# Performance work log

Measured on AMD Instinct MI355X. Metric: run time of the kernel, lower is better.

The kernel has to match this reference:

```python
import jax, jax.numpy as jnp
import numpy as np

B, T, D = 4, 4096, 1024

def setup_inputs() -> dict:
    key = jax.random.key(0)
    kx, kq, kk, kv = jax.random.split(key, 4)
    s = 1.0 / np.sqrt(D)
    return {
        "x": jax.random.normal(kx, (B, T, D), dtype=jnp.float32),
        "Wq": jax.random.normal(kq, (D, D), dtype=jnp.float32) * s,
        "Wk": jax.random.normal(kk, (D, D), dtype=jnp.float32) * s,
        "Wv": jax.random.normal(kv, (D, D), dtype=jnp.float32) * s,
    }

def reference(x, Wq, Wk, Wv):
    # x: [B, T, D]; W*: [D, D] (torch Linear weight, y = x @ W.T)
    Q = jnp.einsum("btd,ed->bte", x, Wq)
    K = jnp.einsum("btd,ed->bte", x, Wk)
    V = jnp.einsum("btd,ed->bte", x, Wv)
    scale = jnp.asarray(np.sqrt(D), dtype=x.dtype)
    scores = jnp.einsum("bqd,bkd->bqk", Q, K) / scale  # [B, T, T]
    weights = jax.nn.softmax(scores, axis=-1)
    return jnp.einsum("bqk,bkd->bqd", weights, V)
```

## Files before the change

### kernel.cpp

```cpp
#include <hip/hip_runtime.h>
#include <stdint.h>

typedef unsigned short u16;
typedef __attribute__((ext_vector_type(4))) float f32x4;
typedef __attribute__((ext_vector_type(8))) short s16x8;

#define TB 4
#define TT 4096
#define TD 1024

__device__ __forceinline__ u16 f2bf(float f) {
  union { float f; uint32_t u; } v; v.f = f;
  return (u16)((v.u + 0x7FFFu + ((v.u >> 16) & 1u)) >> 16);
}

#define GLOAD_LDS16(g, l) __builtin_amdgcn_global_load_lds( \
    (const __attribute__((address_space(1))) void*)(g),      \
    (__attribute__((address_space(3))) void*)(l), 16, 0, 0)

#define MFMA16(a, b, c) __builtin_amdgcn_mfma_f32_16x16x32_bf16(a, b, c, 0, 0, 0)
#define LDSV(o) (*(const s16x8*)&ls[(o)])

__global__ void cast_all(const float* __restrict__ x, const float* __restrict__ wq,
                         const float* __restrict__ wk, const float* __restrict__ wv,
                         u16* __restrict__ dst) {
  const int NX = 1 << 22;
  const int NW = 1 << 18;
  const int NT = NX + 3 * NW;
  int i = blockIdx.x * blockDim.x + threadIdx.x;
  int stride = gridDim.x * blockDim.x;
  for (; i < NT; i += stride) {
    float4 v;
    if (i < NX) {
      v = ((const float4*)x)[i];
    } else {
      int j = i - NX;
      int w = j >> 18;
      int off = j & (NW - 1);
      const float* p = (w == 0) ? wq : (w == 1) ? wk : wv;
      v = ((const float4*)p)[off];
    }
    ushort4 o;
    o.x = f2bf(v.x); o.y = f2bf(v.y); o.z = f2bf(v.z); o.w = f2bf(v.w);
    ((ushort4*)dst)[i] = o;
  }
}

__global__ void zero_l(float* __restrict__ L) {
  ((float4*)L)[blockIdx.x * 256 + threadIdx.x] = (float4){0.f, 0.f, 0.f, 0.f};
}

template<int EPI>
__global__ __launch_bounds__(512)
void gemm256(const u16* __restrict__ Abase, const u16* __restrict__ Bt,
             void* __restrict__ C, float* __restrict__ L,
             int K, int lda, int ldb, int ldc,
             float s0, float s1,
             size_t oA0, size_t oA1, size_t oA2, size_t oA3, size_t sB,
             size_t oC0, size_t oC1, size_t oC2, size_t oC3) {
  __shared__ u16 ls[65536];
  const int tid  = threadIdx.x;
  const int lane = tid & 63;
  const int wid  = tid >> 6;
  const int wm   = wid >> 2;
  const int wn   = wid & 3;

  const int nxy = gridDim.x * gridDim.y;
  const int id  = blockIdx.y * gridDim.x + blockIdx.x;
  const int sid = (id & 7) * (nxy >> 3) + (id >> 3);
  const int bx  = sid % gridDim.x;
  const int by  = sid / gridDim.x;
  const int brow = by * 256;
  const int bcol = bx * 256;

  const int z = blockIdx.z;
  const size_t oA = (z == 0) ? oA0 : (z == 1) ? oA1 : (z == 2) ? oA2 : oA3;
  const size_t oC = (z == 0) ? oC0 : (z == 1) ? oC1 : (z == 2) ? oC2 : oC3;
  const float scale = (z == 0) ? s0 : s1;
  const u16* A = Abase + oA;
  Bt += (size_t)z * sB;

  const int lr = lane >> 3;
  const int lc = (lane & 7) ^ lr;

  auto SBLK = [&](int slotB, int kt, int op, int r0) {
    const u16* g = op ? (Bt + (size_t)bcol * ldb) : (A + (size_t)brow * lda);
    const int ld = op ? ldb : lda;
    const int r  = r0 + wid * 8 + lr;
    GLOAD_LDS16(g + (size_t)r * ld + (size_t)kt * 64 + (size_t)lc * 8,
                &ls[slotB + op * 16384 + (r0 + wid * 8) * 64]);
  };
  auto SHALF = [&](int slotB, int kt, int op, int h) {
    SBLK(slotB, kt, op, h * 128);
    SBLK(slotB, kt, op, h * 128 + 64);
  };

  f32x4 acc[8][4];
#pragma unroll
  for (int m = 0; m < 8; ++m)
#pragma unroll
    for (int n = 0; n < 4; ++n) acc[m][n] = (f32x4){0.f, 0.f, 0.f, 0.f};

  const int nt = K >> 6;
  const int NI = nt >> 1;

  SHALF(0, 0, 0, 0); SHALF(0, 0, 0, 1);
  SHALF(0, 0, 1, 0); SHALF(0, 0, 1, 1);
  SHALF(32768, 1, 1, 0); SHALF(32768, 1, 1, 1);
  asm volatile("s_waitcnt vmcnt(4)" ::: "memory");
  __builtin_amdgcn_s_barrier();

  const int r16 = lane & 15;
  const int k8  = lane >> 4;
  const int sw  = r16 & 7;
  const int c0  = ((k8)     ^ sw) * 8;
  const int c1  = ((4 | k8) ^ sw) * 8;
  int aBase[8], bBase[4];
#pragma unroll
  for (int m = 0; m < 8; ++m) aBase[m] = (wm * 128 + m * 16 + r16) * 64;
#pragma unroll
  for (int n = 0; n < 4; ++n) bBase[n] = 16384 + (wn * 64 + n * 16 + r16) * 64;

  s16x8 af[4][2], bf[4][2];

#define READ_A4(SB, MH)                                                        \
  af[0][0] = LDSV((SB) + aBase[(MH)*4+0] + c0); af[0][1] = LDSV((SB) + aBase[(MH)*4+0] + c1); \
  af[1][0] = LDSV((SB) + aBase[(MH)*4+1] + c0); af[1][1] = LDSV((SB) + aBase[(MH)*4+1] + c1); \
  af[2][0] = LDSV((SB) + aBase[(MH)*4+2] + c0); af[2][1] = LDSV((SB) + aBase[(MH)*4+2] + c1); \
  af[3][0] = LDSV((SB) + aBase[(MH)*4+3] + c0); af[3][1] = LDSV((SB) + aBase[(MH)*4+3] + c1);

#define READ_B2(SB, N0)                                                        \
  bf[(N0)  ][0] = LDSV((SB) + bBase[(N0)  ] + c0); bf[(N0)  ][1] = LDSV((SB) + bBase[(N0)  ] + c1); \
  bf[(N0)+1][0] = LDSV((SB) + bBase[(N0)+1] + c0); bf[(N0)+1][1] = LDSV((SB) + bBase[(N0)+1] + c1);

#define CLUST(MH, NH)                                                          \
  __builtin_amdgcn_s_setprio(1);                                               \
  _Pragma("unroll")                                                            \
  for (int mm = 0; mm < 4; ++mm) {                                             \
    _Pragma("unroll")                                                          \
    for (int nn = 0; nn < 2; ++nn) {                                           \
      acc[(MH)*4+mm][(NH)*2+nn] =                                              \
          MFMA16(af[mm][0], bf[(NH)*2+nn][0], acc[(MH)*4+mm][(NH)*2+nn]);      \
      acc[(MH)*4+mm][(NH)*2+nn] =                                              \
          MFMA16(af[mm][1], bf[(NH)*2+nn][1], acc[(MH)*4+mm][(NH)*2+nn]);      \
    }                                                                          \
  }                                                                            \
  __builtin_amdgcn_s_setprio(0);

#define PIN() __builtin_amdgcn_sched_barrier(0)
#define BAR() __builtin_amdgcn_s_barrier()

  for (int i = 0; i < NI; ++i) {
    const int t1 = 2 * i + 1, t2 = 2 * i + 2, t3 = 2 * i + 3;
    const bool p2 = t2 < nt, p3 = t3 < nt;

    READ_A4(0, 0); READ_B2(0, 0);
    SHALF(32768, t1, 0, 0);
    PIN(); BAR();
    CLUST(0, 0);
    BAR();

    READ_B2(0, 2);
    SHALF(32768, t1, 0, 1);
    PIN(); BAR();
    CLUST(0, 1);
    BAR();

    READ_A4(0, 1);
    if (p2) SHALF(0, t2, 1, 0);
    PIN(); BAR();
    CLUST(1, 0);
    BAR();

    if (p2) SHALF(0, t2, 1, 1);
    PIN(); BAR();
    CLUST(1, 1);
    if (p2) asm volatile("s_waitcnt vmcnt(4)" ::: "memory");
    else    asm volatile("s_waitcnt vmcnt(0)" ::: "memory");
    BAR();

    READ_A4(32768, 0); READ_B2(32768, 0);
    if (p2) SHALF(0, t2, 0, 0);
    PIN(); BAR();
    CLUST(0, 0);
    BAR();

    READ_B2(32768, 2);
    if (p2) SHALF(0, t2, 0, 1);
    PIN(); BAR();
    CLUST(0, 1);
    BAR();

    READ_A4(32768, 1);
    if (p3) SHALF(32768, t3, 1, 0);
    PIN(); BAR();
    CLUST(1, 0);
    BAR();

    if (p3) SHALF(32768, t3, 1, 1);
    PIN(); BAR();
    CLUST(1, 1);
    if (i + 1 < NI) asm volatile("s_waitcnt vmcnt(4)" ::: "memory");
    BAR();
  }
#undef READ_A4
#undef READ_B2
#undef CLUST
#undef PIN
#undef BAR

  const int c16 = lane & 15;
  const int rhi = lane >> 4;
#pragma unroll
  for (int m = 0; m < 8; ++m) {
#pragma unroll
    for (int r = 0; r < 4; ++r) {
      const int grow = brow + wm * 128 + m * 16 + rhi * 4 + r;
      if (EPI == 1) {
        float vs[4];
        float s = 0.f;
#pragma unroll
        for (int n = 0; n < 4; ++n) {
          vs[n] = __expf(acc[m][n][r] * scale);
          s += vs[n];
        }
#pragma unroll
        for (int n = 0; n < 4; ++n) {
          int gcol = bcol + wn * 64 + n * 16 + c16;
          ((u16*)C)[oC + (size_t)grow * ldc + gcol] = f2bf(vs[n]);
        }
#pragma unroll
        for (int off = 1; off < 16; off <<= 1) s += __shfl_xor(s, off);
        if (c16 == 0) atomicAdd(&L[(size_t)z * 4096 + grow], s);
      } else if (EPI == 2) {
        const float inv = 1.0f / L[(size_t)z * 4096 + grow];
#pragma unroll
        for (int n = 0; n < 4; ++n) {
          int gcol = bcol + wn * 64 + n * 16 + c16;
          ((float*)C)[oC + (size_t)grow * ldc + gcol] = acc[m][n][r] * scale * inv;
        }
      } else {
#pragma unroll
        for (int n = 0; n < 4; ++n) {
          int gcol = bcol + wn * 64 + n * 16 + c16;
          ((u16*)C)[oC + (size_t)grow * ldc + gcol] = f2bf(acc[m][n][r] * scale);
        }
      }
    }
  }
}

__global__ __launch_bounds__(256)
void transpose_bf16(const u16* __restrict__ V, u16* __restrict__ Vt) {
  __shared__ u16 tile[64][65];
  int b  = blockIdx.z;
  int t0 = blockIdx.y * 64;
  int e0 = blockIdx.x * 64;
  const u16* Vb  = V  + (size_t)b * TT * TD;
  u16*       Vtb = Vt + (size_t)b * TT * TD;
  int r  = threadIdx.x >> 4;
  int c4 = threadIdx.x & 15;
#pragma unroll
  for (int i = 0; i < 4; ++i) {
    int row = r + i * 16;
    ushort4 v = *(const ushort4*)&Vb[(size_t)(t0 + row) * TD + e0 + c4 * 4];
    tile[row][c4 * 4 + 0] = v.x;
    tile[row][c4 * 4 + 1] = v.y;
    tile[row][c4 * 4 + 2] = v.z;
    tile[row][c4 * 4 + 3] = v.w;
  }
  __syncthreads();
#pragma unroll
  for (int i = 0; i < 4; ++i) {
    int e = r + i * 16;
    ushort4 o;
    o.x = tile[c4 * 4 + 0][e];
    o.y = tile[c4 * 4 + 1][e];
    o.z = tile[c4 * 4 + 2][e];
    o.w = tile[c4 * 4 + 3][e];
    *(ushort4*)&Vtb[(size_t)(e0 + e) * TT + t0 + c4 * 4] = o;
  }
}

extern "C" void kernel_launch(void* const* d_in, const int* in_sizes, int n_in,
                              void* d_out, int out_size, void* d_ws, size_t ws_size,
                              hipStream_t stream) {
  const float* x  = (const float*)d_in[0];
  const float* Wq = (const float*)d_in[1];
  const float* Wk = (const float*)d_in[2];
  const float* Wv = (const float*)d_in[3];
  float* out = (float*)d_out;

  const size_t MT = (size_t)TB * TT;
  const size_t BE = (size_t)TT * TD;
  const size_t XE = MT * TD;
  const size_t WE = (size_t)TD * TD;

  u16* xb   = (u16*)d_ws;
  u16* wqb  = xb + XE;
  u16* Q    = wqb + 3 * WE;
  u16* Kb   = Q + XE;
  u16* Vt   = Kb + XE;
  u16* PB   = Vt + XE;
  u16* tmpS = PB + 2 * XE;
  float* L  = (float*)wqb;

  cast_all<<<2048, 256, 0, stream>>>(x, Wq, Wk, Wv, xb);

  dim3 blk(512);
  gemm256<0><<<dim3(TD / 256, MT / 256, 3), blk, 0, stream>>>(
      xb, wqb, Q, L, TD, TD, TD, TD, 0.03125f, 1.0f,
      0, 0, 0, 0, WE,
      0, XE, (size_t)(PB - Q), 0);

  transpose_bf16<<<dim3(TD / 64, TT / 64, TB), 256, 0, stream>>>(PB, Vt);

  zero_l<<<16, 256, 0, stream>>>(L);

  gemm256<1><<<dim3(TT / 256, TT / 256, TB), blk, 0, stream>>>(
      Q, Kb, xb, L, TD, TD, TD, TT, 1.0f, 1.0f,
      0, BE, 2 * BE, 3 * BE, BE,
      0, (size_t)(PB - xb), (size_t)(PB + XE - xb), (size_t)(tmpS - xb));

  gemm256<2><<<dim3(TD / 256, TT / 256, TB), blk, 0, stream>>>(
      xb, Vt, out, L, TT, TT, TT, TD, 1.0f, 1.0f,
      0, (size_t)(PB - xb), (size_t)(PB + XE - xb), (size_t)(tmpS - xb), BE,
      0, BE, 2 * BE, 3 * BE);
}
```

Baseline: 418.2 us.

## Compute V transposed directly via swapped GEMM and add LDS waitcnt hints

Replaces the V projection followed by a separate bf16 transpose kernel with a GEMM that computes Wv·xᵀ directly into the transposed Vt layout, one batch per grid z. This removes the transpose launch and the write and re-read of the intermediate V buffer. It also inserts explicit lgkmcnt(8) waits before the barriers in the main loop to order the LDS reads against the compute clusters. The swapped-operand GEMM must produce a correct layout through its offsets, and the extra waits could add stalls.

Result: no change. 420.0 us (median of 3 runs) (+0.4%).

```diff
diff --git a/kernel.cpp b/kernel.cpp
--- a/kernel.cpp
+++ b/kernel.cpp
@@ -149,6 +149,7 @@
 
 #define PIN() __builtin_amdgcn_sched_barrier(0)
 #define BAR() __builtin_amdgcn_s_barrier()
+#define LGKM8() asm volatile("s_waitcnt lgkmcnt(8)" ::: "memory")
 
   for (int i = 0; i < NI; ++i) {
     const int t1 = 2 * i + 1, t2 = 2 * i + 2, t3 = 2 * i + 3;
@@ -156,6 +157,7 @@
 
     READ_A4(0, 0); READ_B2(0, 0);
     SHALF(32768, t1, 0, 0);
+    LGKM8();
     PIN(); BAR();
     CLUST(0, 0);
     BAR();
@@ -181,6 +183,7 @@
 
     READ_A4(32768, 0); READ_B2(32768, 0);
     if (p2) SHALF(0, t2, 0, 0);
+    LGKM8();
     PIN(); BAR();
     CLUST(0, 0);
     BAR();
@@ -208,6 +211,7 @@
 #undef CLUST
 #undef PIN
 #undef BAR
+#undef LGKM8
 
   const int c16 = lane & 15;
   const int rhi = lane >> 4;
@@ -247,38 +251,6 @@
         }
       }
     }
-  }
-}
-
-__global__ __launch_bounds__(256)
-void transpose_bf16(const u16* __restrict__ V, u16* __restrict__ Vt) {
-  __shared__ u16 tile[64][65];
-  int b  = blockIdx.z;
-  int t0 = blockIdx.y * 64;
-  int e0 = blockIdx.x * 64;
-  const u16* Vb  = V  + (size_t)b * TT * TD;
-  u16*       Vtb = Vt + (size_t)b * TT * TD;
-  int r  = threadIdx.x >> 4;
-  int c4 = threadIdx.x & 15;
-#pragma unroll
-  for (int i = 0; i < 4; ++i) {
-    int row = r + i * 16;
-    ushort4 v = *(const ushort4*)&Vb[(size_t)(t0 + row) * TD + e0 + c4 * 4];
-    tile[row][c4 * 4 + 0] = v.x;
-    tile[row][c4 * 4 + 1] = v.y;
-    tile[row][c4 * 4 + 2] = v.z;
-    tile[row][c4 * 4 + 3] = v.w;
-  }
-  __syncthreads();
-#pragma unroll
-  for (int i = 0; i < 4; ++i) {
-    int e = r + i * 16;
-    ushort4 o;
-    o.x = tile[c4 * 4 + 0][e];
-    o.y = tile[c4 * 4 + 1][e];
-    o.z = tile[c4 * 4 + 2][e];
-    o.w = tile[c4 * 4 + 3][e];
-    *(ushort4*)&Vtb[(size_t)(e0 + e) * TT + t0 + c4 * 4] = o;
   }
 }
 
@@ -298,6 +270,7 @@
 
   u16* xb   = (u16*)d_ws;
   u16* wqb  = xb + XE;
+  u16* wvb  = wqb + 2 * WE;
   u16* Q    = wqb + 3 * WE;
   u16* Kb   = Q + XE;
   u16* Vt   = Kb + XE;
@@ -308,12 +281,15 @@
   cast_all<<<2048, 256, 0, stream>>>(x, Wq, Wk, Wv, xb);
 
   dim3 blk(512);
-  gemm256<0><<<dim3(TD / 256, MT / 256, 3), blk, 0, stream>>>(
+  gemm256<0><<<dim3(TD / 256, MT / 256, 2), blk, 0, stream>>>(
       xb, wqb, Q, L, TD, TD, TD, TD, 0.03125f, 1.0f,
       0, 0, 0, 0, WE,
-      0, XE, (size_t)(PB - Q), 0);
-
-  transpose_bf16<<<dim3(TD / 64, TT / 64, TB), 256, 0, stream>>>(PB, Vt);
+      0, XE, 0, 0);
+
+  gemm256<0><<<dim3(TT / 256, TD / 256, TB), blk, 0, stream>>>(
+      wvb, xb, Vt, L, TD, TD, TD, TT, 1.0f, 1.0f,
+      0, 0, 0, 0, BE,
+      0, BE, 2 * BE, 3 * BE);
 
   zero_l<<<16, 256, 0, stream>>>(L);
 
```
